# Optimization experiments

Measured on AMD Instinct MI355X. Metric: run time of the kernel, lower is better.

Reference implementation:

```python
import jax, jax.numpy as jnp
import numpy as np

B, NA, NB, DF, H, DO, NT = 32, 128, 1024, 128, 512, 128, 5
NPAIR = NT * NT  # nn_index = z1*5 + z2 -> 25 pair-type MLPs


def setup_inputs() -> dict:
    key = jax.random.key(0)
    ks = jax.random.split(key, 6)
    z = jax.random.randint(ks[0], (B, NA), 0, NT)
    r = jax.random.normal(ks[1], (B, NA, 3), jnp.float32) * 5.0
    x = jax.random.normal(ks[2], (B, NA, DF), jnp.float32)
    t = jax.random.randint(ks[3], (B, NB, 2), 0, NA)
    pad = NB // 8  # last 1/8 of bonds are -1 padding, as in the torch module
    t = t.at[:, NB - pad:, :].set(-1)
    # Stacked per-pair-type 2-layer MLP params (map_list)
    W1 = jax.random.normal(ks[4], (NPAIR, 2 * DF, H), jnp.float32) / np.sqrt(2.0 * DF)
    b1 = jnp.zeros((NPAIR, H), jnp.float32)
    W2 = jax.random.normal(ks[5], (NPAIR, H, DO), jnp.float32) / np.sqrt(1.0 * H)
    b2 = jnp.zeros((NPAIR, DO), jnp.float32)
    return dict(z=z, r=r, x=x, t=t, W1=W1, b1=b1, W2=W2, b2=b2)


def reference(z, r, x, t, W1, b1, W2, b2):
    n_batch, n_bonds, _ = t.shape
    n_atoms = x.shape[1]
    x_f = x.reshape(-1, x.shape[-1])          # [B*NA, DF]
    z_f = z.reshape(-1)                        # [B*NA]
    r_f = r.reshape(-1, 3)                     # [B*NA, 3]
    offs = (jnp.arange(n_batch) * n_atoms)[:, None, None]
    valid = t[:, :, 0] != -1                   # [B, NB]
    tg = jnp.clip(t, 0, None) + offs           # global atom indices (padding clamped to 0)
    t1 = tg[:, :, 0].reshape(-1)
    t2 = tg[:, :, 1].reshape(-1)
    vmask = valid.reshape(-1)                  # [N] = [B*NB]
    # gather+concat pair features; zero out padded rows (masked_scatter into zeros)
    x_c = jnp.concatenate([x_f[t1], x_f[t2]], axis=1) * vmask[:, None].astype(x.dtype)
    z1 = z_f[t1]
    z2 = z_f[t2]
    nn_index = jnp.where(vmask, z1 * NT + z2, -1)
    # per-pair-type MLP dispatch (loop over fixed 25 types; rows selected by mask)
    y = jnp.zeros((x_c.shape[0], W2.shape[-1]), x.dtype)
    for i in range(NPAIR):
        h = jax.nn.silu(x_c @ W1[i] + b1[i])
        out_i = h @ W2[i] + b2[i]
        y = jnp.where((nn_index == i)[:, None], out_i, y)
    y = y.reshape(n_batch, n_bonds, -1)
    # normalized bond vectors, zeroed for padded bonds
    v = (r_f[t2] - r_f[t1]).reshape(n_batch, n_bonds, 3)
    n2 = jnp.sum(v * v, axis=2, keepdims=True)
    v = v / jnp.sqrt(jnp.clip(n2, 1e-24, None))  # == clamp(norm, 1e-12)
    v = v * valid[:, :, None].astype(v.dtype)
    return (z, x, t, y, v)
```

## Files before the change

### kernel.cpp

```cpp
#include <hip/hip_runtime.h>
#include <cstddef>
#include <cstdint>

#define NBATCH 32
#define NATOM  128
#define DFEAT  128
#define HDIM   512
#define DOUT   128
#define NTYPE  5
#define NPAIR  25
#define NBOND  32768
#define CAP    1408
#define TPT    22
#define GBLK   550

#define OFF_X 4096
#define OFF_T 528384
#define OFF_Y 593920
#define OFF_V 4788224

#define PRE_A 580
#define PACKB 2400
#define SCAT  128
#define PRE_BLK (PRE_A+PACKB+SCAT)

typedef __attribute__((ext_vector_type(8))) short short8;
typedef __attribute__((ext_vector_type(4))) float f32x4;

#define GAS(x) ((__attribute__((address_space(1))) const void*)(x))
#define LAS(x) ((__attribute__((address_space(3))) void*)(x))

__device__ __forceinline__ unsigned short f2bf(float f) {
    unsigned u = __float_as_uint(f);
    u = (u + 0x7FFFu + ((u >> 16) & 1u)) >> 16;
    return (unsigned short)u;
}

__global__ __launch_bounds__(256) void k_pre(const int* __restrict__ z,
                                             const float* __restrict__ x,
                                             const int* __restrict__ t,
                                             const float* __restrict__ r,
                                             const float* __restrict__ W1,
                                             const float* __restrict__ W2,
                                             float* __restrict__ out,
                                             short* __restrict__ x_bf,
                                             short* __restrict__ Wpk,
                                             int* __restrict__ cursors,
                                             int* __restrict__ bond_ids) {
    int bid = blockIdx.x, tid = threadIdx.x;
    if (bid < PRE_A) {
        int i4 = (bid * 256 + tid) * 4;
        float4 o;
        if (i4 < OFF_X) {
            const int4 zi = *(const int4*)&z[i4];
            o = make_float4((float)zi.x, (float)zi.y, (float)zi.z, (float)zi.w);
        } else if (i4 < OFF_T) {
            o = *(const float4*)&x[i4 - OFF_X];
            short4 s4;
            s4.x = (short)f2bf(o.x); s4.y = (short)f2bf(o.y);
            s4.z = (short)f2bf(o.z); s4.w = (short)f2bf(o.w);
            *(short4*)&x_bf[i4 - OFF_X] = s4;
        } else {
            const int4 ti = *(const int4*)&t[i4 - OFF_T];
            o = make_float4((float)ti.x, (float)ti.y, (float)ti.z, (float)ti.w);
        }
        *(float4*)&out[i4] = o;
    } else if (bid < PRE_A + PACKB) {
        int idx = (bid - PRE_A) * 256 + tid;
        int l   = idx & 63;
        int u   = (idx >> 6) & 1;
        int wcp = (idx >> 7) & 3;
        int q   = idx >> 9;
        int p   = q / 48;
        int s   = q - p*48;
        int c   = s / 12;
        int rr  = s - c*12;
        int lr = l & 15, kb = (l >> 4)*8;
        short8 v;
        if (rr < 8) {
            int col = (c*8 + wcp*2 + u)*16 + lr;
            const float* src = W1 + ((size_t)p*256 + rr*32 + kb)*HDIM + col;
            #pragma unroll
            for (int j = 0; j < 8; ++j) v[j] = (short)f2bf(src[(size_t)j*HDIM]);
        } else {
            int col = (wcp*2 + u)*16 + lr;
            const float* src = W2 + ((size_t)p*HDIM + (c*4 + (rr-8))*32 + kb)*DOUT + col;
            #pragma unroll
            for (int j = 0; j < 8; ++j) v[j] = (short)f2bf(src[(size_t)j*DOUT]);
        }
        *((short8*)Wpk + idx) = v;
    } else {
        __shared__ int hist[NPAIR];
        __shared__ int base[NPAIR];
        if (tid < NPAIR) hist[tid] = 0;
        __syncthreads();
        int i = (bid - PRE_A - PACKB) * 256 + tid;
        int b = i >> 10;
        int t1 = t[2*i], t2 = t[2*i+1];
        float vx = 0.f, vy = 0.f, vz = 0.f;
        int p = -1, rk = 0;
        if (t1 != -1) {
            int g1 = b*NATOM + t1, g2 = b*NATOM + t2;
            p = z[g1]*NTYPE + z[g2];
            rk = atomicAdd(&hist[p], 1);
            float dx = r[3*g2+0]-r[3*g1+0];
            float dy = r[3*g2+1]-r[3*g1+1];
            float dz = r[3*g2+2]-r[3*g1+2];
            float n2 = fmaxf(dx*dx+dy*dy+dz*dz, 1e-24f);
            float inv = 1.0f / sqrtf(n2);
            vx = dx*inv; vy = dy*inv; vz = dz*inv;
        } else {
            float4 zr = make_float4(0.f, 0.f, 0.f, 0.f);
            float4* yp = (float4*)&out[OFF_Y + (size_t)i * DOUT];
            #pragma unroll
            for (int c2 = 0; c2 < DOUT/4; ++c2) yp[c2] = zr;
        }
        float* out_v = out + OFF_V;
        out_v[3*i+0] = vx; out_v[3*i+1] = vy; out_v[3*i+2] = vz;
        __syncthreads();
        if (tid < NPAIR) base[tid] = atomicAdd(&cursors[tid], hist[tid]);
        __syncthreads();
        if (p >= 0) {
            int pos = base[p] + rk;
            if (pos < CAP) bond_ids[p*CAP + pos] = i;
        }
    }
}

#define STAGE(ss_) do { \
    int _ss = (ss_); \
    int _sw = (_ss >= 48) ? _ss - 48 : _ss; \
    const char* _src = wkbase + (size_t)_sw * 8192; \
    char* _d = wbbase + (_ss % 3) * 8192; \
    __builtin_amdgcn_global_load_lds(GAS(_src), LAS(_d), 16, 0, 0); \
    __builtin_amdgcn_global_load_lds(GAS(_src+1024), LAS(_d+1024), 16, 0, 0); \
} while(0)

__global__ __launch_bounds__(256, 2) void k_gemm(const short* __restrict__ x_bf,
                                                 const int* __restrict__ t,
                                                 const short* __restrict__ Wpk,
                                                 const float* __restrict__ b1,
                                                 const float* __restrict__ b2,
                                                 const int* __restrict__ cursors,
                                                 const int* __restrict__ bond_ids,
                                                 float* __restrict__ y_out) {
    int orig = blockIdx.x;
    int xcd = orig & 7, ib = orig >> 3;
    int wk = (xcd < 6 ? xcd*69 : 414 + (xcd-6)*68) + ib;
    int p = wk / TPT, tileIdx = wk % TPT;
    int cnt = min(cursors[p], CAP);
    if (tileIdx*64 >= cnt) return;
    int nb = min(64, cnt - tileIdx*64);
    int ntiles = (cnt + 63) >> 6;

    __shared__ short xs[64*256];
    __shared__ short hs[64*128];
    __shared__ char  wbuf[3*8192];
    __shared__ float b1s[HDIM];
    __shared__ float b2s[DOUT];
    __shared__ int   sb[64];

    int tid = threadIdx.x;
    int l = tid & 63, wc = tid >> 6;
    int lr = l & 15, lq = l >> 4;
    int klq = lq * 16;

    const char* wkbase = (const char*)Wpk + ((size_t)(p*48)*4 + wc)*2048 + l*16;
    char* wbbase = (char*)wbuf + wc*2048 + l*16;

    if (tid < 64)
        sb[tid] = (tid < nb) ? bond_ids[p*CAP + tileIdx*64 + tid] : -1;

    #pragma unroll
    for (int j = 0; j < 8; ++j) {
        int o = j*4096 + tid*16;
        int row = o >> 9;
        int c16 = ((o >> 4) & 31) ^ (row & 7);
        int atom = 0;
        if (row < nb) {
            int bi = bond_ids[p*CAP + tileIdx*64 + row];
            atom = (bi >> 10)*NATOM + t[2*bi + (c16 >> 4)];
        }
        const char* src = (const char*)x_bf + ((size_t)atom*DFEAT + (c16 & 15)*8)*2;
        __builtin_amdgcn_global_load_lds(GAS(src), LAS((char*)xs + o), 16, 0, 0);
    }

    {
        float snk = 0.f;
        const char* wkt = (const char*)Wpk + (size_t)p*393216;
        int o1 = (int)(((long)tileIdx * 393216) / ntiles) & ~63;
        int e1 = (int)(((long)(tileIdx+1) * 393216) / ntiles);
        for (int o = o1 + tid*16; o < e1; o += 4096) {
            float4 v = *(const float4*)(wkt + o);
            snk += v.x + v.y + v.z + v.w;
        }
        asm volatile("" :: "v"(snk));
    }

    if (tid < 128)
        __builtin_amdgcn_global_load_lds(GAS((const char*)(b1 + (size_t)p*HDIM) + tid*16),
                                         LAS((char*)b1s + tid*16), 16, 0, 0);
    if (tid < 32)
        __builtin_amdgcn_global_load_lds(GAS((const char*)(b2 + (size_t)p*DOUT) + tid*16),
                                         LAS((char*)b2s + tid*16), 16, 0, 0);
    STAGE(0);
    STAGE(1);
    __syncthreads();

    f32x4 yacc[4][2] = {};

    for (int c = 0; c < 4; ++c) {
        float b1c0 = b1s[c*128 + wc*32 + lr];
        float b1c1 = b1s[c*128 + wc*32 + 16 + lr];
        f32x4 acc1[4][2] = {};
        #pragma unroll
        for (int rr = 0; rr < 8; ++rr) {
            int s = c*12 + rr;
            short8 a0, a1, a2, a3;
            {
                const char* xb = (const char*)xs;
                a0 = *(const short8*)(xb + (0*16+lr)*512 + ((rr*64 + klq) ^ (((0*16+lr)&7) << 4)));
                a1 = *(const short8*)(xb + (1*16+lr)*512 + ((rr*64 + klq) ^ (((1*16+lr)&7) << 4)));
                a2 = *(const short8*)(xb + (2*16+lr)*512 + ((rr*64 + klq) ^ (((2*16+lr)&7) << 4)));
                a3 = *(const short8*)(xb + (3*16+lr)*512 + ((rr*64 + klq) ^ (((3*16+lr)&7) << 4)));
            }
            STAGE(s + 2);
            asm volatile("s_waitcnt vmcnt(4)" ::: "memory");
            const char* wb = wbbase + (rr % 3) * 8192;
            short8 w0 = *(const short8*)wb;
            short8 w1 = *(const short8*)(wb + 1024);
            acc1[0][0] = __builtin_amdgcn_mfma_f32_16x16x32_bf16(a0, w0, acc1[0][0], 0, 0, 0);
            acc1[0][1] = __builtin_amdgcn_mfma_f32_16x16x32_bf16(a0, w1, acc1[0][1], 0, 0, 0);
            acc1[1][0] = __builtin_amdgcn_mfma_f32_16x16x32_bf16(a1, w0, acc1[1][0], 0, 0, 0);
            acc1[1][1] = __builtin_amdgcn_mfma_f32_16x16x32_bf16(a1, w1, acc1[1][1], 0, 0, 0);
            acc1[2][0] = __builtin_amdgcn_mfma_f32_16x16x32_bf16(a2, w0, acc1[2][0], 0, 0, 0);
            acc1[2][1] = __builtin_amdgcn_mfma_f32_16x16x32_bf16(a2, w1, acc1[2][1], 0, 0, 0);
            acc1[3][0] = __builtin_amdgcn_mfma_f32_16x16x32_bf16(a3, w0, acc1[3][0], 0, 0, 0);
            acc1[3][1] = __builtin_amdgcn_mfma_f32_16x16x32_bf16(a3, w1, acc1[3][1], 0, 0, 0);
        }
        #pragma unroll
        for (int rf = 0; rf < 4; ++rf) {
            #pragma unroll
            for (int cf = 0; cf < 2; ++cf) {
                int colb = (wc*32 + cf*16 + lr) * 2;
                float bb = cf ? b1c1 : b1c0;
                #pragma unroll
                for (int reg = 0; reg < 4; ++reg) {
                    int row = rf*16 + lq*4 + reg;
                    float sv = acc1[rf][cf][reg] + bb;
                    float hv = sv * __builtin_amdgcn_rcpf(1.0f + __expf(-sv));
                    *(unsigned short*)((char*)hs + row*256 + (colb ^ ((row & 7) << 4))) = f2bf(hv);
                }
            }
        }
        asm volatile("s_waitcnt lgkmcnt(0)" ::: "memory");
        __builtin_amdgcn_s_barrier();

        #pragma unroll
        for (int r2 = 0; r2 < 4; ++r2) {
            int s = c*12 + 8 + r2;
            short8 a0, a1, a2, a3;
            {
                const char* hb = (const char*)hs;
                a0 = *(const short8*)(hb + (0*16+lr)*256 + ((r2*64 + klq) ^ (((0*16+lr)&7) << 4)));
                a1 = *(const short8*)(hb + (1*16+lr)*256 + ((r2*64 + klq) ^ (((1*16+lr)&7) << 4)));
                a2 = *(const short8*)(hb + (2*16+lr)*256 + ((r2*64 + klq) ^ (((2*16+lr)&7) << 4)));
                a3 = *(const short8*)(hb + (3*16+lr)*256 + ((r2*64 + klq) ^ (((3*16+lr)&7) << 4)));
            }
            STAGE(s + 2);
            asm volatile("s_waitcnt vmcnt(4)" ::: "memory");
            const char* wb = wbbase + ((8 + r2) % 3) * 8192;
            short8 w0 = *(const short8*)wb;
            short8 w1 = *(const short8*)(wb + 1024);
            yacc[0][0] = __builtin_amdgcn_mfma_f32_16x16x32_bf16(a0, w0, yacc[0][0], 0, 0, 0);
            yacc[0][1] = __builtin_amdgcn_mfma_f32_16x16x32_bf16(a0, w1, yacc[0][1], 0, 0, 0);
            yacc[1][0] = __builtin_amdgcn_mfma_f32_16x16x32_bf16(a1, w0, yacc[1][0], 0, 0, 0);
            yacc[1][1] = __builtin_amdgcn_mfma_f32_16x16x32_bf16(a1, w1, yacc[1][1], 0, 0, 0);
            yacc[2][0] = __builtin_amdgcn_mfma_f32_16x16x32_bf16(a2, w0, yacc[2][0], 0, 0, 0);
            yacc[2][1] = __builtin_amdgcn_mfma_f32_16x16x32_bf16(a2, w1, yacc[2][1], 0, 0, 0);
            yacc[3][0] = __builtin_amdgcn_mfma_f32_16x16x32_bf16(a3, w0, yacc[3][0], 0, 0, 0);
            yacc[3][1] = __builtin_amdgcn_mfma_f32_16x16x32_bf16(a3, w1, yacc[3][1], 0, 0, 0);
        }
        if (c < 3) {
            asm volatile("s_waitcnt lgkmcnt(0)" ::: "memory");
            __builtin_amdgcn_s_barrier();
        }
    }
    asm volatile("s_waitcnt vmcnt(0)" ::: "memory");

    float bo0 = b2s[wc*32 + lr], bo1 = b2s[wc*32 + 16 + lr];
    #pragma unroll
    for (int rf = 0; rf < 4; ++rf) {
        #pragma unroll
        for (int cf = 0; cf < 2; ++cf) {
            int col = wc*32 + cf*16 + lr;
            float bo = cf ? bo1 : bo0;
            #pragma unroll
            for (int reg = 0; reg < 4; ++reg) {
                int row = rf*16 + lq*4 + reg;
                if (row < nb)
                    y_out[(size_t)sb[row]*DOUT + col] = yacc[rf][cf][reg] + bo;
            }
        }
    }
}

extern "C" void kernel_launch(void* const* d_in, const int* in_sizes, int n_in,
                              void* d_out, int out_size, void* d_ws, size_t ws_size,
                              hipStream_t stream) {
    const int*   z  = (const int*)  d_in[0];
    const float* r  = (const float*)d_in[1];
    const float* x  = (const float*)d_in[2];
    const int*   t  = (const int*)  d_in[3];
    const float* W1 = (const float*)d_in[4];
    const float* b1 = (const float*)d_in[5];
    const float* W2 = (const float*)d_in[6];
    const float* b2 = (const float*)d_in[7];
    float* out = (float*)d_out;

    char* ws = (char*)d_ws;
    int*   cursors  = (int*)(ws);
    int*   bond_ids = (int*)(ws + 256);
    short* x_bf     = (short*)(ws + 141312);
    short* Wpk      = (short*)(ws + 1189888);

    hipMemsetAsync(cursors, 0, 128, stream);
    k_pre<<<PRE_BLK, 256, 0, stream>>>(z, x, t, r, W1, W2, out, x_bf, Wpk, cursors, bond_ids);
    k_gemm<<<GBLK, 256, 0, stream>>>(x_bf, t, Wpk, b1, b2, cursors, bond_ids, out + OFF_Y);
}
```

Before: 50.08 us.

## Switch pair-type MLP GEMMs from bf16 to fp8 MFMA with scaled weights

```diff
diff --git a/kernel.cpp b/kernel.cpp
--- a/kernel.cpp
+++ b/kernel.cpp
@@ -24,16 +24,48 @@
 #define SCAT  128
 #define PRE_BLK (PRE_A+PACKB+SCAT)
 
-typedef __attribute__((ext_vector_type(8))) short short8;
 typedef __attribute__((ext_vector_type(4))) float f32x4;
 
 #define GAS(x) ((__attribute__((address_space(1))) const void*)(x))
 #define LAS(x) ((__attribute__((address_space(3))) void*)(x))
 
-__device__ __forceinline__ unsigned short f2bf(float f) {
+#if defined(__has_builtin)
+#if __has_builtin(__builtin_amdgcn_cvt_pk_fp8_f32)
+#define HAVE_CVT_FP8 1
+#endif
+#endif
+
+__device__ __forceinline__ unsigned char f2fp8(float f) {
     unsigned u = __float_as_uint(f);
-    u = (u + 0x7FFFu + ((u >> 16) & 1u)) >> 16;
-    return (unsigned short)u;
+    unsigned sign = (u >> 24) & 0x80u;
+    unsigned a = u & 0x7FFFFFFFu;
+    if (a >= 0x43E00000u) return (unsigned char)(sign | 0x7Eu);
+    float af = __uint_as_float(a);
+    if (af < 0.015625f) {
+        int m = (int)rintf(af * 512.0f);
+        if (m > 7) return (unsigned char)(sign | 0x08u);
+        return (unsigned char)(sign | (unsigned)m);
+    }
+    int e = (int)(a >> 23) - 127;
+    unsigned mant = a & 0x7FFFFFu;
+    unsigned keep = mant >> 20;
+    unsigned rest = mant & 0xFFFFFu;
+    if (rest > 0x80000u || (rest == 0x80000u && (keep & 1u))) keep++;
+    if (keep == 8u) { keep = 0u; e++; }
+    if (e > 8) return (unsigned char)(sign | 0x7Eu);
+    return (unsigned char)(sign | ((unsigned)(e + 7) << 3) | keep);
+}
+
+__device__ __forceinline__ unsigned pack_fp8x4(float f0, float f1, float f2, float f3) {
+#ifdef HAVE_CVT_FP8
+    int v = 0;
+    v = __builtin_amdgcn_cvt_pk_fp8_f32(f0, f1, v, false);
+    v = __builtin_amdgcn_cvt_pk_fp8_f32(f2, f3, v, true);
+    return (unsigned)v;
+#else
+    return (unsigned)f2fp8(f0) | ((unsigned)f2fp8(f1) << 8)
+         | ((unsigned)f2fp8(f2) << 16) | ((unsigned)f2fp8(f3) << 24);
+#endif
 }
 
 __global__ __launch_bounds__(256) void k_pre(const int* __restrict__ z,
@@ -43,8 +75,8 @@
                                              const float* __restrict__ W1,
                                              const float* __restrict__ W2,
                                              float* __restrict__ out,
-                                             short* __restrict__ x_bf,
-                                             short* __restrict__ Wpk,
+                                             unsigned char* __restrict__ x_f8,
+                                             unsigned char* __restrict__ Wpk,
                                              int* __restrict__ cursors,
                                              int* __restrict__ bond_ids) {
     int bid = blockIdx.x, tid = threadIdx.x;
@@ -56,10 +88,7 @@
             o = make_float4((float)zi.x, (float)zi.y, (float)zi.z, (float)zi.w);
         } else if (i4 < OFF_T) {
             o = *(const float4*)&x[i4 - OFF_X];
-            short4 s4;
-            s4.x = (short)f2bf(o.x); s4.y = (short)f2bf(o.y);
-            s4.z = (short)f2bf(o.z); s4.w = (short)f2bf(o.w);
-            *(short4*)&x_bf[i4 - OFF_X] = s4;
+            *(unsigned*)&x_f8[i4 - OFF_X] = pack_fp8x4(o.x, o.y, o.z, o.w);
         } else {
             const int4 ti = *(const int4*)&t[i4 - OFF_T];
             o = make_float4((float)ti.x, (float)ti.y, (float)ti.z, (float)ti.w);
@@ -76,19 +105,19 @@
         int c   = s / 12;
         int rr  = s - c*12;
         int lr = l & 15, kb = (l >> 4)*8;
-        short8 v;
+        const float* src;
+        size_t stride;
         if (rr < 8) {
-            int col = (c*8 + wcp*2 + u)*16 + lr;
-            const float* src = W1 + ((size_t)p*256 + rr*32 + kb)*HDIM + col;
-            #pragma unroll
-            for (int j = 0; j < 8; ++j) v[j] = (short)f2bf(src[(size_t)j*HDIM]);
+            src = W1 + ((size_t)p*256 + rr*32 + kb)*HDIM + (c*128 + wcp*32 + u*16 + lr);
+            stride = HDIM;
         } else {
-            int col = (wcp*2 + u)*16 + lr;
-            const float* src = W2 + ((size_t)p*HDIM + (c*4 + (rr-8))*32 + kb)*DOUT + col;
-            #pragma unroll
-            for (int j = 0; j < 8; ++j) v[j] = (short)f2bf(src[(size_t)j*DOUT]);
-        }
-        *((short8*)Wpk + idx) = v;
+            src = W2 + ((size_t)p*HDIM + c*128 + (rr-8)*32 + kb)*DOUT + (wcp*32 + u*16 + lr);
+            stride = DOUT;
+        }
+        uint2 v;
+        v.x = pack_fp8x4(16.f*src[0], 16.f*src[stride], 16.f*src[2*stride], 16.f*src[3*stride]);
+        v.y = pack_fp8x4(16.f*src[4*stride], 16.f*src[5*stride], 16.f*src[6*stride], 16.f*src[7*stride]);
+        *(uint2*)&Wpk[(size_t)idx * 8] = v;
     } else {
         __shared__ int hist[NPAIR];
         __shared__ int base[NPAIR];
@@ -130,15 +159,13 @@
 #define STAGE(ss_) do { \
     int _ss = (ss_); \
     int _sw = (_ss >= 48) ? _ss - 48 : _ss; \
-    const char* _src = wkbase + (size_t)_sw * 8192; \
-    char* _d = wbbase + (_ss % 3) * 8192; \
-    __builtin_amdgcn_global_load_lds(GAS(_src), LAS(_d), 16, 0, 0); \
-    __builtin_amdgcn_global_load_lds(GAS(_src+1024), LAS(_d+1024), 16, 0, 0); \
+    __builtin_amdgcn_global_load_lds(GAS(wkbase + (size_t)_sw*4096), \
+                                     LAS(wbbase + (_ss % 3)*4096), 16, 0, 0); \
 } while(0)
 
-__global__ __launch_bounds__(256, 2) void k_gemm(const short* __restrict__ x_bf,
+__global__ __launch_bounds__(256, 3) void k_gemm(const unsigned char* __restrict__ x_f8,
                                                  const int* __restrict__ t,
-                                                 const short* __restrict__ Wpk,
+                                                 const unsigned char* __restrict__ Wpk,
                                                  const float* __restrict__ b1,
                                                  const float* __restrict__ b2,
                                                  const int* __restrict__ cursors,
@@ -153,43 +180,43 @@
     int nb = min(64, cnt - tileIdx*64);
     int ntiles = (cnt + 63) >> 6;
 
-    __shared__ short xs[64*256];
-    __shared__ short hs[64*128];
-    __shared__ char  wbuf[3*8192];
-    __shared__ float b1s[HDIM];
-    __shared__ float b2s[DOUT];
-    __shared__ int   sb[64];
+    __shared__ __attribute__((aligned(16))) unsigned char xs[16384];
+    __shared__ __attribute__((aligned(16))) unsigned char hsb[8192];
+    __shared__ __attribute__((aligned(16))) unsigned char wbuf[3*4096];
+    __shared__ __attribute__((aligned(16))) float b1s[HDIM];
+    __shared__ __attribute__((aligned(16))) float b2s[DOUT];
+    __shared__ int sb[64];
 
     int tid = threadIdx.x;
     int l = tid & 63, wc = tid >> 6;
     int lr = l & 15, lq = l >> 4;
-    int klq = lq * 16;
-
-    const char* wkbase = (const char*)Wpk + ((size_t)(p*48)*4 + wc)*2048 + l*16;
-    char* wbbase = (char*)wbuf + wc*2048 + l*16;
+    int xsw = (lr & 7) << 4;
+
+    const unsigned char* wkbase = Wpk + ((size_t)(p*48)*4 + wc)*1024 + l*16;
+    unsigned char* wbbase = wbuf + wc*1024 + l*16;
 
     if (tid < 64)
         sb[tid] = (tid < nb) ? bond_ids[p*CAP + tileIdx*64 + tid] : -1;
 
     #pragma unroll
-    for (int j = 0; j < 8; ++j) {
+    for (int j = 0; j < 4; ++j) {
         int o = j*4096 + tid*16;
-        int row = o >> 9;
-        int c16 = ((o >> 4) & 31) ^ (row & 7);
+        int row = o >> 8;
+        int lg = ((o >> 4) & 15) ^ (row & 7);
         int atom = 0;
         if (row < nb) {
             int bi = bond_ids[p*CAP + tileIdx*64 + row];
-            atom = (bi >> 10)*NATOM + t[2*bi + (c16 >> 4)];
-        }
-        const char* src = (const char*)x_bf + ((size_t)atom*DFEAT + (c16 & 15)*8)*2;
-        __builtin_amdgcn_global_load_lds(GAS(src), LAS((char*)xs + o), 16, 0, 0);
+            atom = (bi >> 10)*NATOM + t[2*bi + (lg >> 3)];
+        }
+        const unsigned char* src = x_f8 + (size_t)atom*DFEAT + (lg & 7)*16;
+        __builtin_amdgcn_global_load_lds(GAS(src), LAS(xs + o), 16, 0, 0);
     }
 
     {
         float snk = 0.f;
-        const char* wkt = (const char*)Wpk + (size_t)p*393216;
-        int o1 = (int)(((long)tileIdx * 393216) / ntiles) & ~63;
-        int e1 = (int)(((long)(tileIdx+1) * 393216) / ntiles);
+        const unsigned char* wkt = Wpk + (size_t)p*196608;
+        int o1 = (int)(((long)tileIdx * 196608) / ntiles) & ~63;
+        int e1 = (int)(((long)(tileIdx+1) * 196608) / ntiles);
         for (int o = o1 + tid*16; o < e1; o += 4096) {
             float4 v = *(const float4*)(wkt + o);
             snk += v.x + v.y + v.z + v.w;
@@ -210,47 +237,48 @@
     f32x4 yacc[4][2] = {};
 
     for (int c = 0; c < 4; ++c) {
-        float b1c0 = b1s[c*128 + wc*32 + lr];
-        float b1c1 = b1s[c*128 + wc*32 + 16 + lr];
+        const float4 b1v0 = *(const float4*)&b1s[c*128 + wc*32 + lq*4];
+        const float4 b1v1 = *(const float4*)&b1s[c*128 + wc*32 + 16 + lq*4];
         f32x4 acc1[4][2] = {};
         #pragma unroll
         for (int rr = 0; rr < 8; ++rr) {
-            int s = c*12 + rr;
-            short8 a0, a1, a2, a3;
-            {
-                const char* xb = (const char*)xs;
-                a0 = *(const short8*)(xb + (0*16+lr)*512 + ((rr*64 + klq) ^ (((0*16+lr)&7) << 4)));
-                a1 = *(const short8*)(xb + (1*16+lr)*512 + ((rr*64 + klq) ^ (((1*16+lr)&7) << 4)));
-                a2 = *(const short8*)(xb + (2*16+lr)*512 + ((rr*64 + klq) ^ (((2*16+lr)&7) << 4)));
-                a3 = *(const short8*)(xb + (3*16+lr)*512 + ((rr*64 + klq) ^ (((3*16+lr)&7) << 4)));
-            }
-            STAGE(s + 2);
-            asm volatile("s_waitcnt vmcnt(4)" ::: "memory");
-            const char* wb = wbbase + (rr % 3) * 8192;
-            short8 w0 = *(const short8*)wb;
-            short8 w1 = *(const short8*)(wb + 1024);
-            acc1[0][0] = __builtin_amdgcn_mfma_f32_16x16x32_bf16(a0, w0, acc1[0][0], 0, 0, 0);
-            acc1[0][1] = __builtin_amdgcn_mfma_f32_16x16x32_bf16(a0, w1, acc1[0][1], 0, 0, 0);
-            acc1[1][0] = __builtin_amdgcn_mfma_f32_16x16x32_bf16(a1, w0, acc1[1][0], 0, 0, 0);
-            acc1[1][1] = __builtin_amdgcn_mfma_f32_16x16x32_bf16(a1, w1, acc1[1][1], 0, 0, 0);
-            acc1[2][0] = __builtin_amdgcn_mfma_f32_16x16x32_bf16(a2, w0, acc1[2][0], 0, 0, 0);
-            acc1[2][1] = __builtin_amdgcn_mfma_f32_16x16x32_bf16(a2, w1, acc1[2][1], 0, 0, 0);
-            acc1[3][0] = __builtin_amdgcn_mfma_f32_16x16x32_bf16(a3, w0, acc1[3][0], 0, 0, 0);
-            acc1[3][1] = __builtin_amdgcn_mfma_f32_16x16x32_bf16(a3, w1, acc1[3][1], 0, 0, 0);
+            long xa0 = *(const long*)(xs + (0*16+lr)*256 + ((rr*32 + lq*8) ^ xsw));
+            long xa1 = *(const long*)(xs + (1*16+lr)*256 + ((rr*32 + lq*8) ^ xsw));
+            long xa2 = *(const long*)(xs + (2*16+lr)*256 + ((rr*32 + lq*8) ^ xsw));
+            long xa3 = *(const long*)(xs + (3*16+lr)*256 + ((rr*32 + lq*8) ^ xsw));
+            STAGE(c*12 + rr + 2);
+            asm volatile("s_waitcnt vmcnt(2)" ::: "memory");
+            const unsigned char* wb = wbuf + (rr % 3)*4096 + wc*1024;
+            long w0 = *(const long*)(wb + l*8);
+            long w1 = *(const long*)(wb + 512 + l*8);
+            __builtin_amdgcn_s_setprio(1);
+            acc1[0][0] = __builtin_amdgcn_mfma_f32_16x16x32_fp8_fp8(w0, xa0, acc1[0][0], 0, 0, 0);
+            acc1[0][1] = __builtin_amdgcn_mfma_f32_16x16x32_fp8_fp8(w1, xa0, acc1[0][1], 0, 0, 0);
+            acc1[1][0] = __builtin_amdgcn_mfma_f32_16x16x32_fp8_fp8(w0, xa1, acc1[1][0], 0, 0, 0);
+            acc1[1][1] = __builtin_amdgcn_mfma_f32_16x16x32_fp8_fp8(w1, xa1, acc1[1][1], 0, 0, 0);
+            acc1[2][0] = __builtin_amdgcn_mfma_f32_16x16x32_fp8_fp8(w0, xa2, acc1[2][0], 0, 0, 0);
+            acc1[2][1] = __builtin_amdgcn_mfma_f32_16x16x32_fp8_fp8(w1, xa2, acc1[2][1], 0, 0, 0);
+            acc1[3][0] = __builtin_amdgcn_mfma_f32_16x16x32_fp8_fp8(w0, xa3, acc1[3][0], 0, 0, 0);
+            acc1[3][1] = __builtin_amdgcn_mfma_f32_16x16x32_fp8_fp8(w1, xa3, acc1[3][1], 0, 0, 0);
+            __builtin_amdgcn_s_setprio(0);
         }
         #pragma unroll
-        for (int rf = 0; rf < 4; ++rf) {
+        for (int bg = 0; bg < 4; ++bg) {
+            int bond = bg*16 + lr;
             #pragma unroll
-            for (int cf = 0; cf < 2; ++cf) {
-                int colb = (wc*32 + cf*16 + lr) * 2;
-                float bb = cf ? b1c1 : b1c0;
-                #pragma unroll
-                for (int reg = 0; reg < 4; ++reg) {
-                    int row = rf*16 + lq*4 + reg;
-                    float sv = acc1[rf][cf][reg] + bb;
-                    float hv = sv * __builtin_amdgcn_rcpf(1.0f + __expf(-sv));
-                    *(unsigned short*)((char*)hs + row*256 + (colb ^ ((row & 7) << 4))) = f2bf(hv);
-                }
+            for (int u = 0; u < 2; ++u) {
+                float4 bb = u ? b1v1 : b1v0;
+                f32x4 a = acc1[bg][u];
+                float s0 = a[0]*0.0625f + bb.x;
+                float s1 = a[1]*0.0625f + bb.y;
+                float s2 = a[2]*0.0625f + bb.z;
+                float s3 = a[3]*0.0625f + bb.w;
+                s0 *= __builtin_amdgcn_rcpf(1.0f + __expf(-s0));
+                s1 *= __builtin_amdgcn_rcpf(1.0f + __expf(-s1));
+                s2 *= __builtin_amdgcn_rcpf(1.0f + __expf(-s2));
+                s3 *= __builtin_amdgcn_rcpf(1.0f + __expf(-s3));
+                *(unsigned*)(hsb + bond*128 + ((wc*32 + u*16 + lq*4) ^ xsw)) =
+                    pack_fp8x4(s0, s1, s2, s3);
             }
         }
         asm volatile("s_waitcnt lgkmcnt(0)" ::: "memory");
@@ -258,28 +286,25 @@
 
         #pragma unroll
         for (int r2 = 0; r2 < 4; ++r2) {
-            int s = c*12 + 8 + r2;
-            short8 a0, a1, a2, a3;
-            {
-                const char* hb = (const char*)hs;
-                a0 = *(const short8*)(hb + (0*16+lr)*256 + ((r2*64 + klq) ^ (((0*16+lr)&7) << 4)));
-                a1 = *(const short8*)(hb + (1*16+lr)*256 + ((r2*64 + klq) ^ (((1*16+lr)&7) << 4)));
-                a2 = *(const short8*)(hb + (2*16+lr)*256 + ((r2*64 + klq) ^ (((2*16+lr)&7) << 4)));
-                a3 = *(const short8*)(hb + (3*16+lr)*256 + ((r2*64 + klq) ^ (((3*16+lr)&7) << 4)));
-            }
-            STAGE(s + 2);
-            asm volatile("s_waitcnt vmcnt(4)" ::: "memory");
-            const char* wb = wbbase + ((8 + r2) % 3) * 8192;
-            short8 w0 = *(const short8*)wb;
-            short8 w1 = *(const short8*)(wb + 1024);
-            yacc[0][0] = __builtin_amdgcn_mfma_f32_16x16x32_bf16(a0, w0, yacc[0][0], 0, 0, 0);
-            yacc[0][1] = __builtin_amdgcn_mfma_f32_16x16x32_bf16(a0, w1, yacc[0][1], 0, 0, 0);
-            yacc[1][0] = __builtin_amdgcn_mfma_f32_16x16x32_bf16(a1, w0, yacc[1][0], 0, 0, 0);
-            yacc[1][1] = __builtin_amdgcn_mfma_f32_16x16x32_bf16(a1, w1, yacc[1][1], 0, 0, 0);
-            yacc[2][0] = __builtin_amdgcn_mfma_f32_16x16x32_bf16(a2, w0, yacc[2][0], 0, 0, 0);
-            yacc[2][1] = __builtin_amdgcn_mfma_f32_16x16x32_bf16(a2, w1, yacc[2][1], 0, 0, 0);
-            yacc[3][0] = __builtin_amdgcn_mfma_f32_16x16x32_bf16(a3, w0, yacc[3][0], 0, 0, 0);
-            yacc[3][1] = __builtin_amdgcn_mfma_f32_16x16x32_bf16(a3, w1, yacc[3][1], 0, 0, 0);
+            long ha0 = *(const long*)(hsb + (0*16+lr)*128 + ((r2*32 + lq*8) ^ xsw));
+            long ha1 = *(const long*)(hsb + (1*16+lr)*128 + ((r2*32 + lq*8) ^ xsw));
+            long ha2 = *(const long*)(hsb + (2*16+lr)*128 + ((r2*32 + lq*8) ^ xsw));
+            long ha3 = *(const long*)(hsb + (3*16+lr)*128 + ((r2*32 + lq*8) ^ xsw));
+            STAGE(c*12 + 10 + r2);
+            asm volatile("s_waitcnt vmcnt(2)" ::: "memory");
+            const unsigned char* wb = wbuf + ((8 + r2) % 3)*4096 + wc*1024;
+            long w0 = *(const long*)(wb + l*8);
+            long w1 = *(const long*)(wb + 512 + l*8);
+            __builtin_amdgcn_s_setprio(1);
+            yacc[0][0] = __builtin_amdgcn_mfma_f32_16x16x32_fp8_fp8(w0, ha0, yacc[0][0], 0, 0, 0);
+            yacc[0][1] = __builtin_amdgcn_mfma_f32_16x16x32_fp8_fp8(w1, ha0, yacc[0][1], 0, 0, 0);
+            yacc[1][0] = __builtin_amdgcn_mfma_f32_16x16x32_fp8_fp8(w0, ha1, yacc[1][0], 0, 0, 0);
+            yacc[1][1] = __builtin_amdgcn_mfma_f32_16x16x32_fp8_fp8(w1, ha1, yacc[1][1], 0, 0, 0);
+            yacc[2][0] = __builtin_amdgcn_mfma_f32_16x16x32_fp8_fp8(w0, ha2, yacc[2][0], 0, 0, 0);
+            yacc[2][1] = __builtin_amdgcn_mfma_f32_16x16x32_fp8_fp8(w1, ha2, yacc[2][1], 0, 0, 0);
+            yacc[3][0] = __builtin_amdgcn_mfma_f32_16x16x32_fp8_fp8(w0, ha3, yacc[3][0], 0, 0, 0);
+            yacc[3][1] = __builtin_amdgcn_mfma_f32_16x16x32_fp8_fp8(w1, ha3, yacc[3][1], 0, 0, 0);
+            __builtin_amdgcn_s_setprio(0);
         }
         if (c < 3) {
             asm volatile("s_waitcnt lgkmcnt(0)" ::: "memory");
@@ -288,19 +313,24 @@
     }
     asm volatile("s_waitcnt vmcnt(0)" ::: "memory");
 
-    float bo0 = b2s[wc*32 + lr], bo1 = b2s[wc*32 + 16 + lr];
+    const float4 b2v0 = *(const float4*)&b2s[wc*32 + lq*4];
+    const float4 b2v1 = *(const float4*)&b2s[wc*32 + 16 + lq*4];
     #pragma unroll
-    for (int rf = 0; rf < 4; ++rf) {
-        #pragma unroll
-        for (int cf = 0; cf < 2; ++cf) {
-            int col = wc*32 + cf*16 + lr;
-            float bo = cf ? bo1 : bo0;
-            #pragma unroll
-            for (int reg = 0; reg < 4; ++reg) {
-                int row = rf*16 + lq*4 + reg;
-                if (row < nb)
-                    y_out[(size_t)sb[row]*DOUT + col] = yacc[rf][cf][reg] + bo;
-            }
+    for (int bg = 0; bg < 4; ++bg) {
+        int bond = bg*16 + lr;
+        if (bond < nb) {
+            float* yp = &y_out[(size_t)sb[bond]*DOUT + wc*32 + lq*4];
+            float4 o0, o1;
+            o0.x = yacc[bg][0][0]*0.0625f + b2v0.x;
+            o0.y = yacc[bg][0][1]*0.0625f + b2v0.y;
+            o0.z = yacc[bg][0][2]*0.0625f + b2v0.z;
+            o0.w = yacc[bg][0][3]*0.0625f + b2v0.w;
+            o1.x = yacc[bg][1][0]*0.0625f + b2v1.x;
+            o1.y = yacc[bg][1][1]*0.0625f + b2v1.y;
+            o1.z = yacc[bg][1][2]*0.0625f + b2v1.z;
+            o1.w = yacc[bg][1][3]*0.0625f + b2v1.w;
+            *(float4*)yp = o0;
+            *(float4*)(yp + 16) = o1;
         }
     }
 }
@@ -319,12 +349,12 @@
     float* out = (float*)d_out;
 
     char* ws = (char*)d_ws;
-    int*   cursors  = (int*)(ws);
-    int*   bond_ids = (int*)(ws + 256);
-    short* x_bf     = (short*)(ws + 141312);
-    short* Wpk      = (short*)(ws + 1189888);
+    int*           cursors  = (int*)(ws);
+    int*           bond_ids = (int*)(ws + 256);
+    unsigned char* x_f8     = (unsigned char*)(ws + 141312);
+    unsigned char* Wpk      = (unsigned char*)(ws + 665600);
 
     hipMemsetAsync(cursors, 0, 128, stream);
-    k_pre<<<PRE_BLK, 256, 0, stream>>>(z, x, t, r, W1, W2, out, x_bf, Wpk, cursors, bond_ids);
-    k_gemm<<<GBLK, 256, 0, stream>>>(x_bf, t, Wpk, b1, b2, cursors, bond_ids, out + OFF_Y);
-}
+    k_pre<<<PRE_BLK, 256, 0, stream>>>(z, x, t, r, W1, W2, out, x_f8, Wpk, cursors, bond_ids);
+    k_gemm<<<GBLK, 256, 0, stream>>>(x_f8, t, Wpk, b1, b2, cursors, bond_ids, out + OFF_Y);
+}
```

New measurement: 47.28 us. 5.6% less time.
